# Kernel tuning notes

Measured on AMD Instinct MI355X. Metric: run time of the kernel, lower is better.

Reference implementation:

```python
import jax, jax.numpy as jnp
import numpy as np

D_MODEL, D_STATE, EXPAND = 1024, 64, 2
D_INNER = EXPAND * D_MODEL
BATCH, SEQ = 4, 2048


def setup_inputs() -> dict:
    key = jax.random.key(0)
    ks = jax.random.split(key, 7)
    s = lambda *d: 1.0 / np.sqrt(d[0])
    x = jax.random.normal(ks[0], (BATCH, SEQ, D_MODEL), dtype=jnp.float32)
    # weights stored as [in, out] so y = x @ W
    W_in = jax.random.normal(ks[1], (D_MODEL, 2 * D_INNER), dtype=jnp.float32) * s(D_MODEL)
    W_xp = jax.random.normal(ks[2], (D_INNER, 2 * D_STATE + 1), dtype=jnp.float32) * s(D_INNER)
    W_B = jax.random.normal(ks[3], (D_STATE, D_INNER), dtype=jnp.float32) * s(D_STATE)
    W_C = jax.random.normal(ks[4], (D_STATE, D_INNER), dtype=jnp.float32) * s(D_STATE)
    W_out = jax.random.normal(ks[5], (D_INNER, D_MODEL), dtype=jnp.float32) * s(D_INNER)
    D = jnp.ones((D_INNER,), dtype=jnp.float32)
    A_log = jnp.asarray(np.log(0.01), dtype=jnp.float32)
    return {"x": x, "W_in": W_in, "W_xp": W_xp, "W_B": W_B,
            "W_C": W_C, "W_out": W_out, "D": D, "A_log": A_log}


def _scan_recurrence(a, b):
    """h_t = a_t * h_{t-1} + b_t via associative scan over seq axis (axis=1).
    a, b: [B, S, D_inner]."""
    def combine(e1, e2):
        a1, b1 = e1
        a2, b2 = e2
        return a1 * a2, a2 * b1 + b2
    _, h = jax.lax.associative_scan(combine, (a, b), axis=1)
    return h


def reference(x, W_in, W_xp, W_B, W_C, W_out, D, A_log):
    xz = x @ W_in                               # [B,S,2*Di]
    xi, z = jnp.split(xz, 2, axis=-1)           # each [B,S,Di]
    proj = xi @ W_xp                            # [B,S,2*Ds+1]
    delta = jax.nn.softplus(proj[..., :1])      # [B,S,1]
    B_raw = proj[..., 1:1 + D_STATE]
    C_raw = proj[..., 1 + D_STATE:]
    B = B_raw @ W_B                             # [B,S,Di]
    C = C_raw @ W_C                             # [B,S,Di]
    A = -jnp.exp(A_log)                         # scalar
    A_bar = jnp.exp(delta * A)                  # [B,S,1]
    a = jnp.broadcast_to(A_bar, B.shape)        # [B,S,Di]
    h = _scan_recurrence(a, B * xi)             # [B,S,Di]
    y = C * h + D * xi                          # [B,S,Di]
    y = y * jax.nn.silu(z)
    return y @ W_out                            # [B,S,Dm]
```

## Files before the change

### kernel.cpp

```cpp
#include <hip/hip_runtime.h>
#include <hip/hip_bf16.h>
#include <cstdint>
#include <cstddef>

#define D_MODEL 1024
#define D_STATE 64
#define D_INNER 2048
#define BATCH   4
#define SEQ     2048
#define MROWS   (BATCH*SEQ)
#define CHUNK   32
#define NCHUNK  (SEQ/CHUNK)

typedef __bf16 bf16x8 __attribute__((ext_vector_type(8)));
typedef float  f32x4  __attribute__((ext_vector_type(4)));

__device__ __forceinline__ float bf2f(unsigned short u) {
    union { unsigned int i; float f; } v; v.i = ((unsigned int)u) << 16; return v.f;
}
__device__ __forceinline__ unsigned short f2bf(float f) {
    union { float f; unsigned int i; } v; v.f = f;
    unsigned int r = v.i + 0x7fff + ((v.i >> 16) & 1);
    return (unsigned short)(r >> 16);
}
__device__ __forceinline__ float lo16(unsigned u){ return bf2f((unsigned short)(u & 0xffffu)); }
__device__ __forceinline__ float hi16(unsigned u){ return bf2f((unsigned short)(u >> 16)); }
__device__ __forceinline__ unsigned pack2(float a, float b){
    return (unsigned)f2bf(a) | ((unsigned)f2bf(b) << 16);
}

__global__ __launch_bounds__(256) void f32_to_bf16(const float* __restrict__ in,
                                                   unsigned short* __restrict__ out) {
    size_t i = ((size_t)blockIdx.x * 256 + threadIdx.x) * 4;
    float4 v = *(const float4*)(in + i);
    uint2 o; o.x = pack2(v.x, v.y); o.y = pack2(v.z, v.w);
    *(uint2*)(out + i) = o;
}

__global__ void transpose_f32_bf16(const float* __restrict__ in,
                                   unsigned short* __restrict__ out, int rows, int cols) {
    __shared__ float t[32][33];
    int bx = blockIdx.x * 32, by = blockIdx.y * 32;
    int tx = threadIdx.x, ty = threadIdx.y;
    int r = by + ty, c = bx + tx;
    if (r < rows && c < cols) t[ty][tx] = in[(size_t)r * cols + c];
    __syncthreads();
    int ro = bx + ty, co = by + tx;
    if (ro < cols && co < rows) out[(size_t)ro * rows + co] = f2bf(t[tx][ty]);
}

__global__ void transpose_wxp(const float* __restrict__ wxp,
                              unsigned short* __restrict__ out) {
    __shared__ float t[32][33];
    int j0 = blockIdx.x * 32, k0 = blockIdx.y * 32;
    int tx = threadIdx.x, ty = threadIdx.y;
    t[ty][tx] = wxp[(size_t)(k0 + ty) * 129 + 1 + j0 + tx];
    __syncthreads();
    out[(size_t)(j0 + ty) * 2048 + k0 + tx] = f2bf(t[tx][ty]);
}

__global__ void extract_w0(const float* __restrict__ wxp, float* __restrict__ w0f) {
    int k = blockIdx.x * 256 + threadIdx.x;
    if (k < D_INNER) w0f[k] = wxp[(size_t)k * 129];
}

#define BM 128
#define BN 128
enum { EPI_PLAIN = 0, EPI_MUL_XI = 2, EPI_F32OUT = 3, EPI_F32ACC = 4 };

__device__ __forceinline__ void gload_lds16(const void* g, void* l) {
    __builtin_amdgcn_global_load_lds((const __attribute__((address_space(1))) void*)g,
                                     (__attribute__((address_space(3))) void*)l, 16, 0, 0);
}

template<int EPI>
__global__ __launch_bounds__(256) void gemm_tn(
    const unsigned short* __restrict__ A,
    const unsigned short* __restrict__ BT,
    void* __restrict__ Cv,
    const unsigned short* __restrict__ XI, int ldxi,
    int M, int N, int kchunk, int lda, int ldb, int ldc)
{
    __shared__ __align__(16) unsigned short As0[BM * 32];
    __shared__ __align__(16) unsigned short As1[BM * 32];
    __shared__ __align__(16) unsigned short Bs0[BN * 32];
    __shared__ __align__(16) unsigned short Bs1[BN * 32];
    const int tid  = threadIdx.x;
    const int wave = tid >> 6, lane = tid & 63;
    const int row0 = blockIdx.y * BM, col0 = blockIdx.x * BN;
    const int wr = (wave >> 1) * 64, wc = (wave & 1) * 64;
    const int srow = lane >> 2;
    const int scol = (lane & 3) * 8;

    f32x4 acc[4][4];
    #pragma unroll
    for (int i = 0; i < 4; ++i)
        #pragma unroll
        for (int j = 0; j < 4; ++j)
            #pragma unroll
            for (int r = 0; r < 4; ++r) acc[i][j][r] = 0.0f;

    const int kbeg = blockIdx.z * kchunk;
    for (int k0 = kbeg; k0 < kbeg + kchunk; k0 += 64) {
        #pragma unroll
        for (int qi = 0; qi < 2; ++qi) {
            int q = wave * 2 + qi;
            const unsigned short* gA = A  + (size_t)(row0 + q*16 + srow) * lda + (k0 + scol);
            const unsigned short* gB = BT + (size_t)(col0 + q*16 + srow) * ldb + (k0 + scol);
            gload_lds16(gA,      &As0[q * 512]);
            gload_lds16(gA + 32, &As1[q * 512]);
            gload_lds16(gB,      &Bs0[q * 512]);
            gload_lds16(gB + 32, &Bs1[q * 512]);
        }
        __syncthreads();
        bf16x8 af0[4], af1[4], bf0[4], bf1[4];
        const int lro = lane & 15, lko = (lane >> 4) * 8;
        #pragma unroll
        for (int t = 0; t < 4; ++t) {
            af0[t] = *(const bf16x8*)&As0[(wr + t*16 + lro) * 32 + lko];
            af1[t] = *(const bf16x8*)&As1[(wr + t*16 + lro) * 32 + lko];
            bf0[t] = *(const bf16x8*)&Bs0[(wc + t*16 + lro) * 32 + lko];
            bf1[t] = *(const bf16x8*)&Bs1[(wc + t*16 + lro) * 32 + lko];
        }
        #pragma unroll
        for (int i = 0; i < 4; ++i)
            #pragma unroll
            for (int j = 0; j < 4; ++j) {
                acc[i][j] = __builtin_amdgcn_mfma_f32_16x16x32_bf16(af0[i], bf0[j], acc[i][j], 0, 0, 0);
                acc[i][j] = __builtin_amdgcn_mfma_f32_16x16x32_bf16(af1[i], bf1[j], acc[i][j], 0, 0, 0);
            }
        __syncthreads();
    }

    const int r0 = (lane >> 4) * 4, cl = lane & 15;
    #pragma unroll
    for (int i = 0; i < 4; ++i) {
        #pragma unroll
        for (int j = 0; j < 4; ++j) {
            #pragma unroll
            for (int r = 0; r < 4; ++r) {
                int gr = row0 + wr + i*16 + r0 + r;
                int gc = col0 + wc + j*16 + cl;
                float v = acc[i][j][r];
                if (EPI == EPI_MUL_XI) v *= bf2f(XI[(size_t)gr * ldxi + gc]);
                if (EPI == EPI_F32OUT)      ((float*)Cv)[(size_t)gr * ldc + gc] = v;
                else if (EPI == EPI_F32ACC) ((float*)Cv + (size_t)blockIdx.z * M * ldc)[(size_t)gr * ldc + gc] = v;
                else                        ((unsigned short*)Cv)[(size_t)gr * ldc + gc] = f2bf(v);
            }
        }
    }
}

__global__ __launch_bounds__(256) void reduce_proj(const float* __restrict__ part,
                                                   unsigned short* __restrict__ out) {
    size_t i = ((size_t)blockIdx.x * 256 + threadIdx.x) * 4;
    const size_t stride = (size_t)MROWS * 128;
    float4 s = *(const float4*)(part + i);
    #pragma unroll
    for (int p = 1; p < 4; ++p) {
        float4 v = *(const float4*)(part + p * stride + i);
        s.x += v.x; s.y += v.y; s.z += v.z; s.w += v.w;
    }
    uint2 o; o.x = pack2(s.x, s.y); o.y = pack2(s.z, s.w);
    *(uint2*)(out + i) = o;
}

__global__ __launch_bounds__(256) void delta_kernel(
    const unsigned short* __restrict__ xz, const float* __restrict__ w0f,
    const float* __restrict__ A_log,
    float* __restrict__ dA, float* __restrict__ abar)
{
    int row  = blockIdx.x * 4 + (threadIdx.x >> 6);
    int lane = threadIdx.x & 63;
    const unsigned short* xi = xz + (size_t)row * (2 * D_INNER);
    float s = 0.f;
    #pragma unroll
    for (int step = 0; step < 4; ++step) {
        int oct = step * 64 + lane;
        uint4 u = *(const uint4*)(xi + oct * 8);
        const float4* pw = (const float4*)(w0f + oct * 8);
        float4 wa = pw[0], wb = pw[1];
        s += lo16(u.x)*wa.x + hi16(u.x)*wa.y + lo16(u.y)*wa.z + hi16(u.y)*wa.w
           + lo16(u.z)*wb.x + hi16(u.z)*wb.y + lo16(u.w)*wb.z + hi16(u.w)*wb.w;
    }
    #pragma unroll
    for (int off = 32; off > 0; off >>= 1) s += __shfl_xor(s, off);
    if (lane == 0) {
        float Av = -expf(A_log[0]);
        float d  = (s > 20.f) ? s : log1pf(expf(s));
        float da = d * Av;
        dA[row] = da;
        abar[row] = expf(da);
    }
}

__global__ void chunk_prod(const float* __restrict__ dA, float* __restrict__ P) {
    int idx = threadIdx.x;
    float s = 0.f;
    #pragma unroll
    for (int t = 0; t < CHUNK; ++t) s += dA[idx * CHUNK + t];
    P[idx] = expf(s);
}

__global__ __launch_bounds__(256) void scan_local(
    const unsigned short* __restrict__ bxi, const float* __restrict__ abar,
    float* __restrict__ carry)
{
    int cb = blockIdx.x, j = blockIdx.y, b = blockIdx.z;
    int c0 = cb * 1024 + threadIdx.x * 4;
    int srow = b * SEQ + j * CHUNK;
    const float* ab = abar + srow;
    const unsigned short* p = bxi + (size_t)srow * D_INNER + c0;
    float h0 = 0.f, h1 = 0.f, h2 = 0.f, h3 = 0.f;
    #pragma unroll 8
    for (int t = 0; t < CHUNK; ++t) {
        float a = ab[t];
        uint2 u = *(const uint2*)(p + (size_t)t * D_INNER);
        h0 = fmaf(a, h0, lo16(u.x)); h1 = fmaf(a, h1, hi16(u.x));
        h2 = fmaf(a, h2, lo16(u.y)); h3 = fmaf(a, h3, hi16(u.y));
    }
    *(float4*)(carry + ((size_t)(b * NCHUNK + j)) * D_INNER + c0) = make_float4(h0, h1, h2, h3);
}

__global__ __launch_bounds__(256) void scan_chunks(float* __restrict__ carry,
                                                   const float* __restrict__ P) {
    int c = blockIdx.x * 256 + threadIdx.x;
    int b = blockIdx.y;
    float H = 0.f;
    for (int j = 0; j < NCHUNK; ++j) {
        size_t idx = ((size_t)(b * NCHUNK + j)) * D_INNER + c;
        float cr = carry[idx];
        carry[idx] = H;
        H = P[b * NCHUNK + j] * H + cr;
    }
}

__global__ __launch_bounds__(256) void scan_final(
    const unsigned short* bxi, const unsigned short* __restrict__ cmat,
    const unsigned short* __restrict__ xz, const float* __restrict__ Dvf,
    const float* __restrict__ abar, const float* __restrict__ carry,
    unsigned short* ypre)
{
    int cb = blockIdx.x, j = blockIdx.y, b = blockIdx.z;
    int c0 = cb * 1024 + threadIdx.x * 4;
    int srow = b * SEQ + j * CHUNK;
    float4 hin = *(const float4*)(carry + ((size_t)(b * NCHUNK + j)) * D_INNER + c0);
    float h0 = hin.x, h1 = hin.y, h2 = hin.z, h3 = hin.w;
    float4 dv = *(const float4*)(Dvf + c0);
    float d0 = dv.x, d1 = dv.y, d2 = dv.z, d3 = dv.w;
    const float* ab = abar + srow;
    #pragma unroll 4
    for (int t = 0; t < CHUNK; ++t) {
        size_t m = (size_t)(srow + t);
        float a = ab[t];
        uint2 ub = *(const uint2*)(bxi + m * D_INNER + c0);
        h0 = fmaf(a, h0, lo16(ub.x)); h1 = fmaf(a, h1, hi16(ub.x));
        h2 = fmaf(a, h2, lo16(ub.y)); h3 = fmaf(a, h3, hi16(ub.y));
        uint2 uc = *(const uint2*)(cmat + m * D_INNER + c0);
        uint2 ux = *(const uint2*)(xz + m * (2 * D_INNER) + c0);
        uint2 uz = *(const uint2*)(xz + m * (2 * D_INNER) + D_INNER + c0);
        float y0 = lo16(uc.x) * h0 + d0 * lo16(ux.x);
        float y1 = hi16(uc.x) * h1 + d1 * hi16(ux.x);
        float y2 = lo16(uc.y) * h2 + d2 * lo16(ux.y);
        float y3 = hi16(uc.y) * h3 + d3 * hi16(ux.y);
        float z0 = lo16(uz.x), z1 = hi16(uz.x), z2 = lo16(uz.y), z3 = hi16(uz.y);
        y0 *= z0 / (1.f + expf(-z0)); y1 *= z1 / (1.f + expf(-z1));
        y2 *= z2 / (1.f + expf(-z2)); y3 *= z3 / (1.f + expf(-z3));
        uint2 o; o.x = pack2(y0, y1); o.y = pack2(y2, y3);
        *(uint2*)(ypre + m * D_INNER + c0) = o;
    }
}

extern "C" void kernel_launch(void* const* d_in, const int* in_sizes, int n_in,
                              void* d_out, int out_size, void* d_ws, size_t ws_size,
                              hipStream_t stream) {
    const float* x     = (const float*)d_in[0];
    const float* W_in  = (const float*)d_in[1];
    const float* W_xp  = (const float*)d_in[2];
    const float* W_B   = (const float*)d_in[3];
    const float* W_C   = (const float*)d_in[4];
    const float* W_out = (const float*)d_in[5];
    const float* Dv    = (const float*)d_in[6];
    const float* A_log = (const float*)d_in[7];
    float* out = (float*)d_out;

    size_t off = 0;
    auto alloc = [&](size_t bytes) {
        void* p = (char*)d_ws + off; off += (bytes + 255) & ~(size_t)255; return p;
    };
    unsigned short* xbf   = (unsigned short*)alloc((size_t)MROWS * D_MODEL * 2);
    unsigned short* xz    = (unsigned short*)alloc((size_t)MROWS * 2 * D_INNER * 2);
    unsigned short* bxi   = (unsigned short*)alloc((size_t)MROWS * D_INNER * 2);
    unsigned short* cmat  = (unsigned short*)alloc((size_t)MROWS * D_INNER * 2);
    unsigned short* winT  = (unsigned short*)alloc((size_t)4096 * 1024 * 2);
    unsigned short* woutT = (unsigned short*)alloc((size_t)1024 * 2048 * 2);
    unsigned short* wbT   = (unsigned short*)alloc((size_t)2048 * 64 * 2);
    unsigned short* wcT   = (unsigned short*)alloc((size_t)2048 * 64 * 2);
    unsigned short* wxpT  = (unsigned short*)alloc((size_t)128 * 2048 * 2);
    unsigned short* projb = (unsigned short*)alloc((size_t)MROWS * 128 * 2);
    float* proj_part = (float*)alloc((size_t)4 * MROWS * 128 * 4);
    float* w0f   = (float*)alloc(2048 * 4);
    float* dA    = (float*)alloc(MROWS * 4);
    float* abar  = (float*)alloc(MROWS * 4);
    float* P     = (float*)alloc(BATCH * NCHUNK * 4);
    float* carry = (float*)alloc((size_t)BATCH * NCHUNK * D_INNER * 4);
    (void)ws_size; (void)n_in; (void)in_sizes; (void)out_size;

    hipLaunchKernelGGL(f32_to_bf16, dim3((MROWS * D_MODEL) / 1024), dim3(256), 0, stream, x, xbf);

    dim3 tb(32, 32);
    hipLaunchKernelGGL(transpose_f32_bf16, dim3(4096/32, 1024/32), tb, 0, stream, W_in,  winT, 1024, 4096);
    hipLaunchKernelGGL(transpose_f32_bf16, dim3(1024/32, 2048/32), tb, 0, stream, W_out, woutT, 2048, 1024);
    hipLaunchKernelGGL(transpose_f32_bf16, dim3(2048/32, 64/32),   tb, 0, stream, W_B,   wbT, 64, 2048);
    hipLaunchKernelGGL(transpose_f32_bf16, dim3(2048/32, 64/32),   tb, 0, stream, W_C,   wcT, 64, 2048);
    hipLaunchKernelGGL(transpose_wxp, dim3(4, 64), tb, 0, stream, W_xp, wxpT);
    hipLaunchKernelGGL(extract_w0, dim3(8), dim3(256), 0, stream, W_xp, w0f);

    hipLaunchKernelGGL((gemm_tn<EPI_PLAIN>), dim3(4096/BN, MROWS/BM), dim3(256), 0, stream,
                       xbf, winT, (void*)xz, (const unsigned short*)nullptr, 0,
                       MROWS, 4096, 1024, 1024, 1024, 4096);

    hipLaunchKernelGGL(delta_kernel, dim3(MROWS/4), dim3(256), 0, stream, xz, w0f, A_log, dA, abar);

    hipLaunchKernelGGL((gemm_tn<EPI_F32ACC>), dim3(1, MROWS/BM, 4), dim3(256), 0, stream,
                       xz, wxpT, (void*)proj_part, (const unsigned short*)nullptr, 0,
                       MROWS, 128, 512, 2*D_INNER, D_INNER, 128);
    hipLaunchKernelGGL(reduce_proj, dim3((MROWS * 128) / 1024), dim3(256), 0, stream,
                       proj_part, projb);

    hipLaunchKernelGGL((gemm_tn<EPI_MUL_XI>), dim3(D_INNER/BN, MROWS/BM), dim3(256), 0, stream,
                       projb, wbT, (void*)bxi, xz, 2*D_INNER,
                       MROWS, D_INNER, 64, 128, 64, D_INNER);
    hipLaunchKernelGGL((gemm_tn<EPI_PLAIN>), dim3(D_INNER/BN, MROWS/BM), dim3(256), 0, stream,
                       projb + 64, wcT, (void*)cmat, (const unsigned short*)nullptr, 0,
                       MROWS, D_INNER, 64, 128, 64, D_INNER);

    hipLaunchKernelGGL(chunk_prod, dim3(1), dim3(BATCH*NCHUNK), 0, stream, dA, P);
    hipLaunchKernelGGL(scan_local,  dim3(2, NCHUNK, BATCH), dim3(256), 0, stream, bxi, abar, carry);
    hipLaunchKernelGGL(scan_chunks, dim3(D_INNER/256, BATCH), dim3(256), 0, stream, carry, P);
    hipLaunchKernelGGL(scan_final,  dim3(2, NCHUNK, BATCH), dim3(256), 0, stream,
                       bxi, cmat, xz, Dv, abar, carry, bxi );

    hipLaunchKernelGGL((gemm_tn<EPI_F32OUT>), dim3(1024/BN, MROWS/BM), dim3(256), 0, stream,
                       bxi, woutT, (void*)out, (const unsigned short*)nullptr, 0,
                       MROWS, 1024, 2048, D_INNER, D_INNER, 1024);
}
```

Baseline: 363.1 us.

## Fuse B/C projection GEMMs into chunked scan kernels, avoid materializing B and C

```diff
diff --git a/kernel.cpp b/kernel.cpp
--- a/kernel.cpp
+++ b/kernel.cpp
@@ -66,7 +66,7 @@
 
 #define BM 128
 #define BN 128
-enum { EPI_PLAIN = 0, EPI_MUL_XI = 2, EPI_F32OUT = 3, EPI_F32ACC = 4 };
+enum { EPI_PLAIN = 0, EPI_F32OUT = 3, EPI_F32ACC = 4 };
 
 __device__ __forceinline__ void gload_lds16(const void* g, void* l) {
     __builtin_amdgcn_global_load_lds((const __attribute__((address_space(1))) void*)g,
@@ -78,7 +78,6 @@
     const unsigned short* __restrict__ A,
     const unsigned short* __restrict__ BT,
     void* __restrict__ Cv,
-    const unsigned short* __restrict__ XI, int ldxi,
     int M, int N, int kchunk, int lda, int ldb, int ldc)
 {
     __shared__ __align__(16) unsigned short As0[BM * 32];
@@ -142,7 +141,6 @@
                 int gr = row0 + wr + i*16 + r0 + r;
                 int gc = col0 + wc + j*16 + cl;
                 float v = acc[i][j][r];
-                if (EPI == EPI_MUL_XI) v *= bf2f(XI[(size_t)gr * ldxi + gc]);
                 if (EPI == EPI_F32OUT)      ((float*)Cv)[(size_t)gr * ldc + gc] = v;
                 else if (EPI == EPI_F32ACC) ((float*)Cv + (size_t)blockIdx.z * M * ldc)[(size_t)gr * ldc + gc] = v;
                 else                        ((unsigned short*)Cv)[(size_t)gr * ldc + gc] = f2bf(v);
@@ -194,32 +192,106 @@
     }
 }
 
-__global__ void chunk_prod(const float* __restrict__ dA, float* __restrict__ P) {
+__global__ void chunk_aux(const float* __restrict__ dA,
+                          float* __restrict__ sfx, float* __restrict__ P) {
     int idx = threadIdx.x;
-    float s = 0.f;
-    #pragma unroll
-    for (int t = 0; t < CHUNK; ++t) s += dA[idx * CHUNK + t];
-    P[idx] = expf(s);
-}
-
-__global__ __launch_bounds__(256) void scan_local(
-    const unsigned short* __restrict__ bxi, const float* __restrict__ abar,
+    float suf = 0.f;
+    for (int t = CHUNK - 1; t >= 0; --t) {
+        sfx[idx * CHUNK + t] = expf(suf);
+        suf += dA[idx * CHUNK + t];
+    }
+    P[idx] = expf(suf);
+}
+
+#define CB 128
+#define R2 64
+#define PST 136
+
+__global__ __launch_bounds__(256) void bc_carry(
+    const unsigned short* __restrict__ proj,
+    const unsigned short* __restrict__ wbT,
+    const unsigned short* __restrict__ xz,
+    const float* __restrict__ sfx,
     float* __restrict__ carry)
 {
-    int cb = blockIdx.x, j = blockIdx.y, b = blockIdx.z;
-    int c0 = cb * 1024 + threadIdx.x * 4;
-    int srow = b * SEQ + j * CHUNK;
-    const float* ab = abar + srow;
-    const unsigned short* p = bxi + (size_t)srow * D_INNER + c0;
-    float h0 = 0.f, h1 = 0.f, h2 = 0.f, h3 = 0.f;
-    #pragma unroll 8
-    for (int t = 0; t < CHUNK; ++t) {
-        float a = ab[t];
-        uint2 u = *(const uint2*)(p + (size_t)t * D_INNER);
-        h0 = fmaf(a, h0, lo16(u.x)); h1 = fmaf(a, h1, hi16(u.x));
-        h2 = fmaf(a, h2, lo16(u.y)); h3 = fmaf(a, h3, hi16(u.y));
-    }
-    *(float4*)(carry + ((size_t)(b * NCHUNK + j)) * D_INNER + c0) = make_float4(h0, h1, h2, h3);
+    __shared__ unsigned short Ps[R2 * PST];
+    __shared__ unsigned short Xs[R2 * PST];
+    const int cb = blockIdx.x, j2 = blockIdx.y, b = blockIdx.z;
+    const int c0 = cb * CB;
+    const int srow = b * SEQ + j2 * R2;
+    const int tid = threadIdx.x, wave = tid >> 6, lane = tid & 63;
+
+    #pragma unroll
+    for (int i = 0; i < 4; ++i) {
+        int e = i * 2048 + tid * 8, r = e >> 7, c = e & 127;
+        uint4 v = *(const uint4*)(proj + (size_t)(srow + r) * 128 + c);
+        *(uint4*)&Ps[r * PST + c] = v;
+    }
+    #pragma unroll
+    for (int i = 0; i < 4; ++i) {
+        int e = i * 2048 + tid * 8, r = e >> 7, c = e & 127;
+        uint4 v = *(const uint4*)(xz + (size_t)(srow + r) * (2*D_INNER) + c0 + c);
+        *(uint4*)&Xs[r * PST + c] = v;
+    }
+    __syncthreads();
+
+    const int mt0 = (wave >> 1) * 2;
+    const int nb  = (wave & 1) * 64;
+    const int lr = lane & 15, lq = lane >> 4;
+
+    f32x4 acc[2][4];
+    #pragma unroll
+    for (int mi = 0; mi < 2; ++mi)
+        #pragma unroll
+        for (int ni = 0; ni < 4; ++ni)
+            #pragma unroll
+            for (int r = 0; r < 4; ++r) acc[mi][ni][r] = 0.0f;
+
+    #pragma unroll
+    for (int s = 0; s < 2; ++s) {
+        bf16x8 af[2], bfr[4];
+        #pragma unroll
+        for (int mi = 0; mi < 2; ++mi)
+            af[mi] = *(const bf16x8*)&Ps[((mt0+mi)*16 + lr) * PST + s*32 + lq*8];
+        #pragma unroll
+        for (int ni = 0; ni < 4; ++ni)
+            bfr[ni] = *(const bf16x8*)(wbT + (size_t)(c0 + nb + ni*16 + lr) * 64 + s*32 + lq*8);
+        #pragma unroll
+        for (int mi = 0; mi < 2; ++mi)
+            #pragma unroll
+            for (int ni = 0; ni < 4; ++ni)
+                acc[mi][ni] = __builtin_amdgcn_mfma_f32_16x16x32_bf16(af[mi], bfr[ni], acc[mi][ni], 0, 0, 0);
+    }
+
+    float w8[2][4];
+    #pragma unroll
+    for (int mi = 0; mi < 2; ++mi)
+        #pragma unroll
+        for (int r = 0; r < 4; ++r)
+            w8[mi][r] = sfx[srow + (mt0+mi)*16 + lq*4 + r];
+
+    float csum[4];
+    #pragma unroll
+    for (int ni = 0; ni < 4; ++ni) {
+        float s = 0.f;
+        #pragma unroll
+        for (int mi = 0; mi < 2; ++mi)
+            #pragma unroll
+            for (int r = 0; r < 4; ++r) {
+                int row = (mt0+mi)*16 + lq*4 + r;
+                float xv = bf2f(Xs[row * PST + nb + ni*16 + lr]);
+                s += w8[mi][r] * acc[mi][ni][r] * xv;
+            }
+        s += __shfl_xor(s, 16);
+        s += __shfl_xor(s, 32);
+        csum[ni] = s;
+    }
+    if (lane < 16) {
+        int jj = j2 * 2 + (mt0 >> 1);
+        float* dst = carry + ((size_t)(b * NCHUNK + jj)) * D_INNER + c0 + nb;
+        #pragma unroll
+        for (int ni = 0; ni < 4; ++ni) dst[ni*16 + lane] = csum[ni];
+    }
 }
 
 __global__ __launch_bounds__(256) void scan_chunks(float* __restrict__ carry,
@@ -235,39 +307,93 @@
     }
 }
 
-__global__ __launch_bounds__(256) void scan_final(
-    const unsigned short* bxi, const unsigned short* __restrict__ cmat,
-    const unsigned short* __restrict__ xz, const float* __restrict__ Dvf,
-    const float* __restrict__ abar, const float* __restrict__ carry,
-    unsigned short* ypre)
+__global__ __launch_bounds__(256) void bc_scan(
+    const unsigned short* __restrict__ proj,
+    const unsigned short* __restrict__ wbT,
+    const unsigned short* __restrict__ wcT,
+    const unsigned short* __restrict__ xz,
+    const float* __restrict__ Dvf,
+    const float* __restrict__ abar,
+    const float* __restrict__ carry,
+    unsigned short* __restrict__ ypre)
 {
-    int cb = blockIdx.x, j = blockIdx.y, b = blockIdx.z;
-    int c0 = cb * 1024 + threadIdx.x * 4;
-    int srow = b * SEQ + j * CHUNK;
-    float4 hin = *(const float4*)(carry + ((size_t)(b * NCHUNK + j)) * D_INNER + c0);
-    float h0 = hin.x, h1 = hin.y, h2 = hin.z, h3 = hin.w;
-    float4 dv = *(const float4*)(Dvf + c0);
-    float d0 = dv.x, d1 = dv.y, d2 = dv.z, d3 = dv.w;
-    const float* ab = abar + srow;
-    #pragma unroll 4
+    __shared__ unsigned short Ps[R2 * PST];
+    __shared__ unsigned short Bt[R2 * PST];
+    __shared__ unsigned short Ct[R2 * PST];
+    const int cb = blockIdx.x, j2 = blockIdx.y, b = blockIdx.z;
+    const int c0 = cb * CB;
+    const int srow = b * SEQ + j2 * R2;
+    const int tid = threadIdx.x, wave = tid >> 6, lane = tid & 63;
+
+    #pragma unroll
+    for (int i = 0; i < 4; ++i) {
+        int e = i * 2048 + tid * 8, r = e >> 7, c = e & 127;
+        uint4 v = *(const uint4*)(proj + (size_t)(srow + r) * 128 + c);
+        *(uint4*)&Ps[r * PST + c] = v;
+    }
+    __syncthreads();
+
+    const int mt0 = (wave >> 1) * 2;
+    const int nb  = (wave & 1) * 64;
+    const int lr = lane & 15, lq = lane >> 4;
+
+    #pragma unroll
+    for (int mat = 0; mat < 2; ++mat) {
+        const unsigned short* W = mat ? wcT : wbT;
+        unsigned short* dst = mat ? Ct : Bt;
+        const int koff = mat ? 64 : 0;
+        f32x4 acc[2][4];
+        #pragma unroll
+        for (int mi = 0; mi < 2; ++mi)
+            #pragma unroll
+            for (int ni = 0; ni < 4; ++ni)
+                #pragma unroll
+                for (int r = 0; r < 4; ++r) acc[mi][ni][r] = 0.0f;
+        #pragma unroll
+        for (int s = 0; s < 2; ++s) {
+            bf16x8 af[2], bfr[4];
+            #pragma unroll
+            for (int mi = 0; mi < 2; ++mi)
+                af[mi] = *(const bf16x8*)&Ps[((mt0+mi)*16 + lr) * PST + koff + s*32 + lq*8];
+            #pragma unroll
+            for (int ni = 0; ni < 4; ++ni)
+                bfr[ni] = *(const bf16x8*)(W + (size_t)(c0 + nb + ni*16 + lr) * 64 + s*32 + lq*8);
+            #pragma unroll
+            for (int mi = 0; mi < 2; ++mi)
+                #pragma unroll
+                for (int ni = 0; ni < 4; ++ni)
+                    acc[mi][ni] = __builtin_amdgcn_mfma_f32_16x16x32_bf16(af[mi], bfr[ni], acc[mi][ni], 0, 0, 0);
+        }
+        #pragma unroll
+        for (int mi = 0; mi < 2; ++mi)
+            #pragma unroll
+            for (int ni = 0; ni < 4; ++ni)
+                #pragma unroll
+                for (int r = 0; r < 4; ++r) {
+                    int row = (mt0+mi)*16 + lq*4 + r;
+                    dst[row * PST + nb + ni*16 + lr] = f2bf(acc[mi][ni][r]);
+                }
+    }
+    __syncthreads();
+
+    const int c  = tid & 127;
+    const int hh = tid >> 7;
+    const int jj = j2 * 2 + hh;
+    const int r0 = hh * 32;
+    float h  = carry[((size_t)(b * NCHUNK + jj)) * D_INNER + c0 + c];
+    float dv = Dvf[c0 + c];
     for (int t = 0; t < CHUNK; ++t) {
-        size_t m = (size_t)(srow + t);
-        float a = ab[t];
-        uint2 ub = *(const uint2*)(bxi + m * D_INNER + c0);
-        h0 = fmaf(a, h0, lo16(ub.x)); h1 = fmaf(a, h1, hi16(ub.x));
-        h2 = fmaf(a, h2, lo16(ub.y)); h3 = fmaf(a, h3, hi16(ub.y));
-        uint2 uc = *(const uint2*)(cmat + m * D_INNER + c0);
-        uint2 ux = *(const uint2*)(xz + m * (2 * D_INNER) + c0);
-        uint2 uz = *(const uint2*)(xz + m * (2 * D_INNER) + D_INNER + c0);
-        float y0 = lo16(uc.x) * h0 + d0 * lo16(ux.x);
-        float y1 = hi16(uc.x) * h1 + d1 * hi16(ux.x);
-        float y2 = lo16(uc.y) * h2 + d2 * lo16(ux.y);
-        float y3 = hi16(uc.y) * h3 + d3 * hi16(ux.y);
-        float z0 = lo16(uz.x), z1 = hi16(uz.x), z2 = lo16(uz.y), z3 = hi16(uz.y);
-        y0 *= z0 / (1.f + expf(-z0)); y1 *= z1 / (1.f + expf(-z1));
-        y2 *= z2 / (1.f + expf(-z2)); y3 *= z3 / (1.f + expf(-z3));
-        uint2 o; o.x = pack2(y0, y1); o.y = pack2(y2, y3);
-        *(uint2*)(ypre + m * D_INNER + c0) = o;
+        int row = r0 + t;
+        size_t m = (size_t)(srow + row);
+        float a  = abar[m];
+        float xv = bf2f(xz[m * (2*D_INNER) + c0 + c]);
+        float zv = bf2f(xz[m * (2*D_INNER) + D_INNER + c0 + c]);
+        float bv = bf2f(Bt[row * PST + c]);
+        float cv = bf2f(Ct[row * PST + c]);
+        h = fmaf(a, h, bv * xv);
+        float y = cv * h + dv * xv;
+        y *= zv / (1.f + expf(-zv));
+        ypre[m * D_INNER + c0 + c] = f2bf(y);
     }
 }
 
@@ -290,8 +416,7 @@
     };
     unsigned short* xbf   = (unsigned short*)alloc((size_t)MROWS * D_MODEL * 2);
     unsigned short* xz    = (unsigned short*)alloc((size_t)MROWS * 2 * D_INNER * 2);
-    unsigned short* bxi   = (unsigned short*)alloc((size_t)MROWS * D_INNER * 2);
-    unsigned short* cmat  = (unsigned short*)alloc((size_t)MROWS * D_INNER * 2);
+    unsigned short* ypre  = (unsigned short*)alloc((size_t)MROWS * D_INNER * 2);
     unsigned short* winT  = (unsigned short*)alloc((size_t)4096 * 1024 * 2);
     unsigned short* woutT = (unsigned short*)alloc((size_t)1024 * 2048 * 2);
     unsigned short* wbT   = (unsigned short*)alloc((size_t)2048 * 64 * 2);
@@ -302,6 +427,7 @@
     float* w0f   = (float*)alloc(2048 * 4);
     float* dA    = (float*)alloc(MROWS * 4);
     float* abar  = (float*)alloc(MROWS * 4);
+    float* sfx   = (float*)alloc(MROWS * 4);
     float* P     = (float*)alloc(BATCH * NCHUNK * 4);
     float* carry = (float*)alloc((size_t)BATCH * NCHUNK * D_INNER * 4);
     (void)ws_size; (void)n_in; (void)in_sizes; (void)out_size;
@@ -317,31 +443,22 @@
     hipLaunchKernelGGL(extract_w0, dim3(8), dim3(256), 0, stream, W_xp, w0f);
 
     hipLaunchKernelGGL((gemm_tn<EPI_PLAIN>), dim3(4096/BN, MROWS/BM), dim3(256), 0, stream,
-                       xbf, winT, (void*)xz, (const unsigned short*)nullptr, 0,
-                       MROWS, 4096, 1024, 1024, 1024, 4096);
+                       xbf, winT, (void*)xz, MROWS, 4096, 1024, 1024, 1024, 4096);
 
     hipLaunchKernelGGL(delta_kernel, dim3(MROWS/4), dim3(256), 0, stream, xz, w0f, A_log, dA, abar);
+    hipLaunchKernelGGL(chunk_aux, dim3(1), dim3(BATCH*NCHUNK), 0, stream, dA, sfx, P);
 
     hipLaunchKernelGGL((gemm_tn<EPI_F32ACC>), dim3(1, MROWS/BM, 4), dim3(256), 0, stream,
-                       xz, wxpT, (void*)proj_part, (const unsigned short*)nullptr, 0,
-                       MROWS, 128, 512, 2*D_INNER, D_INNER, 128);
+                       xz, wxpT, (void*)proj_part, MROWS, 128, 512, 2*D_INNER, D_INNER, 128);
     hipLaunchKernelGGL(reduce_proj, dim3((MROWS * 128) / 1024), dim3(256), 0, stream,
                        proj_part, projb);
 
-    hipLaunchKernelGGL((gemm_tn<EPI_MUL_XI>), dim3(D_INNER/BN, MROWS/BM), dim3(256), 0, stream,
-                       projb, wbT, (void*)bxi, xz, 2*D_INNER,
-                       MROWS, D_INNER, 64, 128, 64, D_INNER);
-    hipLaunchKernelGGL((gemm_tn<EPI_PLAIN>), dim3(D_INNER/BN, MROWS/BM), dim3(256), 0, stream,
-                       projb + 64, wcT, (void*)cmat, (const unsigned short*)nullptr, 0,
-                       MROWS, D_INNER, 64, 128, 64, D_INNER);
-
-    hipLaunchKernelGGL(chunk_prod, dim3(1), dim3(BATCH*NCHUNK), 0, stream, dA, P);
-    hipLaunchKernelGGL(scan_local,  dim3(2, NCHUNK, BATCH), dim3(256), 0, stream, bxi, abar, carry);
+    hipLaunchKernelGGL(bc_carry, dim3(D_INNER/CB, SEQ/R2, BATCH), dim3(256), 0, stream,
+                       projb, wbT, xz, sfx, carry);
     hipLaunchKernelGGL(scan_chunks, dim3(D_INNER/256, BATCH), dim3(256), 0, stream, carry, P);
-    hipLaunchKernelGGL(scan_final,  dim3(2, NCHUNK, BATCH), dim3(256), 0, stream,
-                       bxi, cmat, xz, Dv, abar, carry, bxi );
+    hipLaunchKernelGGL(bc_scan, dim3(D_INNER/CB, SEQ/R2, BATCH), dim3(256), 0, stream,
+                       projb, wbT, wcT, xz, Dv, abar, carry, ypre);
 
     hipLaunchKernelGGL((gemm_tn<EPI_F32OUT>), dim3(1024/BN, MROWS/BM), dim3(256), 0, stream,
-                       bxi, woutT, (void*)out, (const unsigned short*)nullptr, 0,
-                       MROWS, 1024, 2048, D_INNER, D_INNER, 1024);
-}
+                       ypre, woutT, (void*)out, MROWS, 1024, 2048, D_INNER, D_INNER, 1024);
+}
```

After: 357.6 us. About the same (-1.5%).
